# Kernel tuning notes

Hardware: AMD Instinct MI355X
Metric: run time of the kernel (lower is better)

Reference implementation:

```python
import jax, jax.numpy as jnp
import numpy as np
from jax import lax

B, L, D, F = 32, 512, 256, 256
K = 3
EPS = 1e-5


def _layer_norm(h, g, b):
    mu = jnp.mean(h, axis=-1, keepdims=True)
    var = jnp.var(h, axis=-1, keepdims=True)
    return (h - mu) * lax.rsqrt(var + EPS) * g + b


def _conv1d(h, w, b):
    # h: [B, L, Cin], w: [K, Cin, Cout] -> [B, L, Cout], 'same' padding (pad=1, k=3)
    return lax.conv_general_dilated(h, w, window_strides=(1,), padding=[(1, 1)],
                                    dimension_numbers=('NWC', 'WIO', 'NWC')) + b


def _duration_predictor(x, c1w, c1b, ln1g, ln1b, c2w, c2b, ln2g, ln2b, lw, lb):
    h = jax.nn.relu(_layer_norm(_conv1d(x, c1w, c1b), ln1g, ln1b))
    h = jax.nn.relu(_layer_norm(_conv1d(h, c2w, c2b), ln2g, ln2b))
    d = jax.nn.relu(h @ lw + lb)  # [B, L, 1]
    return d[..., 0]              # [B, L] (squeeze, training mode)


def _expand_one(xb, dur, M):
    # xb: [L, D], dur: [L] int. Repeat row i dur[i] times, zero-pad to M frames.
    cs = jnp.cumsum(dur)                              # [L]
    t = jnp.arange(M)                                 # [M]
    idx = jnp.searchsorted(cs, t, side='right')       # phoneme id per frame
    valid = t < cs[-1]
    out = jnp.take(xb, jnp.clip(idx, 0, xb.shape[0] - 1), axis=0)
    return jnp.where(valid[:, None], out, jnp.zeros((), xb.dtype))


def setup_inputs() -> dict:
    key = jax.random.key(0)
    ks = jax.random.split(key, 8)
    s_c = 1.0 / np.sqrt(K * F)
    s_l = 1.0 / np.sqrt(F)
    return {
        'x': jax.random.normal(ks[0], (B, L, D), jnp.float32),
        'durations': jax.random.randint(ks[1], (B, L), 0, 7),
        'mel_max_length': 4096,
        'conv1_w': jax.random.normal(ks[2], (K, D, F), jnp.float32) * s_c,
        'conv1_b': jnp.zeros((F,), jnp.float32),
        'ln1_g': jnp.ones((F,), jnp.float32),
        'ln1_b': jnp.zeros((F,), jnp.float32),
        'conv2_w': jax.random.normal(ks[3], (K, F, F), jnp.float32) * s_c,
        'conv2_b': jnp.zeros((F,), jnp.float32),
        'ln2_g': jnp.ones((F,), jnp.float32),
        'ln2_b': jnp.zeros((F,), jnp.float32),
        'lin_w': jax.random.normal(ks[4], (F, 1), jnp.float32) * s_l,
        'lin_b': jnp.zeros((1,), jnp.float32),
    }


def reference(x, durations, mel_max_length, conv1_w, conv1_b, ln1_g, ln1_b,
              conv2_w, conv2_b, ln2_g, ln2_b, lin_w, lin_b):
    dur_pred = _duration_predictor(x, conv1_w, conv1_b, ln1_g, ln1_b,
                                   conv2_w, conv2_b, ln2_g, ln2_b, lin_w, lin_b)
    dur = durations.astype(jnp.int32)
    output = jax.vmap(lambda xb, db: _expand_one(xb, db, mel_max_length))(x, dur)
    return output, dur_pred
```

## Files before the change

kernel.cpp:

```cpp
#include <hip/hip_runtime.h>

typedef __attribute__((ext_vector_type(8))) short short8;
typedef __attribute__((ext_vector_type(4))) float f32x4;

#define BATCH 32
#define LSEQ  512
#define DIN   256
#define FDIM  256
#define KTOT  768
#define MT    32
#define BK    32
#define PADA  264

__device__ __forceinline__ short f2bf(float f) {
    union { float f; unsigned u; } v; v.f = f;
    unsigned r = v.u + 0x7FFFu + ((v.u >> 16) & 1u);
    return (short)(r >> 16);
}

__global__ __launch_bounds__(512)
void prep_kernel(const int* __restrict__ dur, int* __restrict__ fidx, int M,
                 const float* __restrict__ w1, const float* __restrict__ w2,
                 short* __restrict__ wt1, short* __restrict__ wt2) {
    __shared__ int s[LSEQ];
    const int t = threadIdx.x, b = blockIdx.x;
    if (b < BATCH) {
        s[t] = dur[b * LSEQ + t];
        __syncthreads();
        for (int off = 1; off < LSEQ; off <<= 1) {
            int v = (t >= off) ? s[t - off] : 0;
            __syncthreads();
            s[t] += v;
            __syncthreads();
        }
        for (int f = t; f < M; f += 512) fidx[b * M + f] = -1;
        __syncthreads();
        int lo = (t == 0) ? 0 : s[t - 1];
        int hi = s[t];
        if (hi > M) hi = M;
        for (int j = lo; j < hi; j++) fidx[b * M + j] = b * LSEQ + t;
    } else {
        const int id = (b - BATCH) * 512 + t;
        const int n = id & 255, k = id >> 8;
        const int dst = (((k >> 5) * FDIM) + n) * BK + (k & 31);
        wt1[dst] = f2bf(w1[id]);
        wt2[dst] = f2bf(w2[id]);
    }
}

template<bool AF32, bool FUSE>
__global__ __launch_bounds__(256)
void conv_ln_expand(const void* __restrict__ Asrc, const short* __restrict__ Bt,
                    const float* __restrict__ cb, const float* __restrict__ g,
                    const float* __restrict__ bta, const float* __restrict__ lw,
                    const float* __restrict__ lb, short* __restrict__ Hout,
                    float* __restrict__ Dout,
                    const float4* __restrict__ x4, const int* __restrict__ fidx,
                    float4* __restrict__ out4, int M, int nexp, int ebase)
{
    __shared__ short As[34][PADA];
    __shared__ float redS[MT][4];
    __shared__ float redQ[MT][4];
    __shared__ float redD[MT][4];
    __shared__ float muS[MT];
    __shared__ float rsS[MT];

    const int tid  = threadIdx.x;
    const int lane = tid & 63;

    if (blockIdx.x < (unsigned)nexp) {
        const int fr = (ebase + blockIdx.x) * 4 + (tid >> 6);
        const int idx = fidx[fr];
        const size_t obase = (size_t)fr * 64 + lane;
        if (idx >= 0) out4[obase] = x4[(size_t)idx * 64 + lane];
        else          out4[obase] = make_float4(0.f, 0.f, 0.f, 0.f);
        return;
    }

    const int cblk = blockIdx.x - nexp;
    const int wave = tid >> 6;
    const int ml   = lane & 15;
    const int q    = lane >> 4;
    const int row0 = cblk * MT;
    const int bb   = row0 >> 9;
    const int r0   = row0 & (LSEQ - 1);

    for (int idx = tid; idx < 34 * 32; idx += 256) {
        const int r = idx >> 5, part = idx & 31;
        const int l2 = r0 + r - 1;
        short8 v = {0, 0, 0, 0, 0, 0, 0, 0};
        if (l2 >= 0 && l2 < LSEQ) {
            const size_t off = ((size_t)(bb * LSEQ + l2)) * DIN + part * 8;
            if (AF32) {
                const float4* s4 = (const float4*)((const float*)Asrc + off);
                float4 u0 = s4[0], u1 = s4[1];
                v[0] = f2bf(u0.x); v[1] = f2bf(u0.y); v[2] = f2bf(u0.z); v[3] = f2bf(u0.w);
                v[4] = f2bf(u1.x); v[5] = f2bf(u1.y); v[6] = f2bf(u1.z); v[7] = f2bf(u1.w);
            } else {
                v = *(const short8*)((const short*)Asrc + off);
            }
        }
        *(short8*)&As[r][part * 8] = v;
    }
    __syncthreads();

    f32x4 acc[2][4];
    #pragma unroll
    for (int mt = 0; mt < 2; mt++)
        #pragma unroll
        for (int nt = 0; nt < 4; nt++)
            #pragma unroll
            for (int r = 0; r < 4; r++)
                acc[mt][nt][r] = 0.f;

    const short* bptr = Bt + (size_t)(wave * 64 + ml) * BK + q * 8;
    #pragma unroll 1
    for (int tap = 0; tap < 3; tap++) {
        #pragma unroll
        for (int cc = 0; cc < 8; cc++) {
            short8 af0 = *(const short8*)&As[ml + tap][cc * 32 + q * 8];
            short8 af1 = *(const short8*)&As[16 + ml + tap][cc * 32 + q * 8];
            short8 b0 = *(const short8*)(bptr + 0 * 16 * BK);
            short8 b1 = *(const short8*)(bptr + 1 * 16 * BK);
            short8 b2 = *(const short8*)(bptr + 2 * 16 * BK);
            short8 b3 = *(const short8*)(bptr + 3 * 16 * BK);
            bptr += FDIM * BK;
            acc[0][0] = __builtin_amdgcn_mfma_f32_16x16x32_bf16(af0, b0, acc[0][0], 0, 0, 0);
            acc[0][1] = __builtin_amdgcn_mfma_f32_16x16x32_bf16(af0, b1, acc[0][1], 0, 0, 0);
            acc[0][2] = __builtin_amdgcn_mfma_f32_16x16x32_bf16(af0, b2, acc[0][2], 0, 0, 0);
            acc[0][3] = __builtin_amdgcn_mfma_f32_16x16x32_bf16(af0, b3, acc[0][3], 0, 0, 0);
            acc[1][0] = __builtin_amdgcn_mfma_f32_16x16x32_bf16(af1, b0, acc[1][0], 0, 0, 0);
            acc[1][1] = __builtin_amdgcn_mfma_f32_16x16x32_bf16(af1, b1, acc[1][1], 0, 0, 0);
            acc[1][2] = __builtin_amdgcn_mfma_f32_16x16x32_bf16(af1, b2, acc[1][2], 0, 0, 0);
            acc[1][3] = __builtin_amdgcn_mfma_f32_16x16x32_bf16(af1, b3, acc[1][3], 0, 0, 0);
        }
    }

    float cbv[4], gv[4], bv[4], lwv[4];
    #pragma unroll
    for (int nt = 0; nt < 4; nt++) {
        const int col = wave * 64 + nt * 16 + ml;
        cbv[nt] = cb[col]; gv[nt] = g[col]; bv[nt] = bta[col];
        lwv[nt] = FUSE ? lw[col] : 0.f;
    }
    #pragma unroll
    for (int mt = 0; mt < 2; mt++)
        #pragma unroll
        for (int nt = 0; nt < 4; nt++)
            #pragma unroll
            for (int r = 0; r < 4; r++)
                acc[mt][nt][r] += cbv[nt];

    #pragma unroll
    for (int mt = 0; mt < 2; mt++)
        #pragma unroll
        for (int r = 0; r < 4; r++) {
            float ps = 0.f, pq = 0.f;
            #pragma unroll
            for (int nt = 0; nt < 4; nt++) { float v = acc[mt][nt][r]; ps += v; pq += v * v; }
            #pragma unroll
            for (int d = 1; d < 16; d <<= 1) { ps += __shfl_xor(ps, d); pq += __shfl_xor(pq, d); }
            if (ml == 0) { const int row = mt * 16 + q * 4 + r; redS[row][wave] = ps; redQ[row][wave] = pq; }
        }
    __syncthreads();
    if (tid < MT) {
        float S = 0.f, Q = 0.f;
        #pragma unroll
        for (int w = 0; w < 4; w++) { S += redS[tid][w]; Q += redQ[tid][w]; }
        const float mu  = S * (1.f / 256.f);
        const float var = Q * (1.f / 256.f) - mu * mu;
        muS[tid] = mu; rsS[tid] = rsqrtf(var + 1e-5f);
    }
    __syncthreads();

    if (!FUSE) {
        #pragma unroll
        for (int mt = 0; mt < 2; mt++)
            #pragma unroll
            for (int r = 0; r < 4; r++) {
                const int row = mt * 16 + q * 4 + r;
                const float mu = muS[row], rs = rsS[row];
                #pragma unroll
                for (int nt = 0; nt < 4; nt++) {
                    const int col = wave * 64 + nt * 16 + ml;
                    float v = (acc[mt][nt][r] - mu) * rs * gv[nt] + bv[nt];
                    v = fmaxf(v, 0.f);
                    Hout[(size_t)(row0 + row) * FDIM + col] = f2bf(v);
                }
            }
    } else {
        #pragma unroll
        for (int mt = 0; mt < 2; mt++)
            #pragma unroll
            for (int r = 0; r < 4; r++) {
                const int row = mt * 16 + q * 4 + r;
                const float mu = muS[row], rs = rsS[row];
                float pd = 0.f;
                #pragma unroll
                for (int nt = 0; nt < 4; nt++) {
                    float v = (acc[mt][nt][r] - mu) * rs * gv[nt] + bv[nt];
                    v = fmaxf(v, 0.f);
                    pd += v * lwv[nt];
                }
                #pragma unroll
                for (int d = 1; d < 16; d <<= 1) pd += __shfl_xor(pd, d);
                if (ml == 0) redD[row][wave] = pd;
            }
        __syncthreads();
        if (tid < MT) {
            float Dv = 0.f;
            #pragma unroll
            for (int w = 0; w < 4; w++) Dv += redD[tid][w];
            Dout[row0 + tid] = fmaxf(Dv + lb[0], 0.f);
        }
    }
}

extern "C" void kernel_launch(void* const* d_in, const int* in_sizes, int n_in,
                              void* d_out, int out_size, void* d_ws, size_t ws_size,
                              hipStream_t stream)
{
    const float* x   = (const float*)d_in[0];
    const int*   dur = (const int*)d_in[1];
    const float* c1w = (const float*)d_in[3];
    const float* c1b = (const float*)d_in[4];
    const float* g1  = (const float*)d_in[5];
    const float* b1  = (const float*)d_in[6];
    const float* c2w = (const float*)d_in[7];
    const float* c2b = (const float*)d_in[8];
    const float* g2  = (const float*)d_in[9];
    const float* b2  = (const float*)d_in[10];
    const float* lw  = (const float*)d_in[11];
    const float* lb  = (const float*)d_in[12];

    const int M = (out_size - BATCH * LSEQ) / (BATCH * DIN);
    float* out     = (float*)d_out;
    float* dur_out = out + (size_t)BATCH * M * DIN;

    char* ws   = (char*)d_ws;
    int*  fidx = (int*)ws;
    short* wt1 = (short*)(ws + (512 << 10));
    short* wt2 = (short*)(ws + (512 << 10) + (384 << 10));
    short* h1  = (short*)(ws + (512 << 10) + 2 * (384 << 10));

    const int NCONV = (BATCH * LSEQ) / MT;
    const int NEXP  = (BATCH * M) / 4;
    const int E1    = NEXP / 2;
    const int E2    = NEXP - E1;

    hipLaunchKernelGGL(prep_kernel, dim3(BATCH + (KTOT * FDIM) / 512), dim3(512), 0, stream,
                       dur, fidx, M, c1w, c2w, wt1, wt2);
    hipLaunchKernelGGL((conv_ln_expand<true, false>), dim3(E1 + NCONV), dim3(256), 0, stream,
                       (const void*)x, wt1, c1b, g1, b1, (const float*)nullptr, (const float*)nullptr,
                       h1, (float*)nullptr,
                       (const float4*)x, fidx, (float4*)d_out, M, E1, 0);
    hipLaunchKernelGGL((conv_ln_expand<false, true>), dim3(E2 + NCONV), dim3(256), 0, stream,
                       (const void*)h1, wt2, c2b, g2, b2, lw, lb,
                       (short*)nullptr, dur_out,
                       (const float4*)x, fidx, (float4*)d_out, M, E2, E1);
}
```

Before: 241.8 us.

## Split expand gather out of conv kernels into dedicated multi-row expand kernel

```diff
diff --git a/kernel.cpp b/kernel.cpp
--- a/kernel.cpp
+++ b/kernel.cpp
@@ -50,13 +50,11 @@
 
 template<bool AF32, bool FUSE>
 __global__ __launch_bounds__(256)
-void conv_ln_expand(const void* __restrict__ Asrc, const short* __restrict__ Bt,
-                    const float* __restrict__ cb, const float* __restrict__ g,
-                    const float* __restrict__ bta, const float* __restrict__ lw,
-                    const float* __restrict__ lb, short* __restrict__ Hout,
-                    float* __restrict__ Dout,
-                    const float4* __restrict__ x4, const int* __restrict__ fidx,
-                    float4* __restrict__ out4, int M, int nexp, int ebase)
+void conv_ln(const void* __restrict__ Asrc, const short* __restrict__ Bt,
+             const float* __restrict__ cb, const float* __restrict__ g,
+             const float* __restrict__ bta, const float* __restrict__ lw,
+             const float* __restrict__ lb, short* __restrict__ Hout,
+             float* __restrict__ Dout)
 {
     __shared__ short As[34][PADA];
     __shared__ float redS[MT][4];
@@ -66,22 +64,11 @@
     __shared__ float rsS[MT];
 
     const int tid  = threadIdx.x;
+    const int wave = tid >> 6;
     const int lane = tid & 63;
-
-    if (blockIdx.x < (unsigned)nexp) {
-        const int fr = (ebase + blockIdx.x) * 4 + (tid >> 6);
-        const int idx = fidx[fr];
-        const size_t obase = (size_t)fr * 64 + lane;
-        if (idx >= 0) out4[obase] = x4[(size_t)idx * 64 + lane];
-        else          out4[obase] = make_float4(0.f, 0.f, 0.f, 0.f);
-        return;
-    }
-
-    const int cblk = blockIdx.x - nexp;
-    const int wave = tid >> 6;
     const int ml   = lane & 15;
     const int q    = lane >> 4;
-    const int row0 = cblk * MT;
+    const int row0 = blockIdx.x * MT;
     const int bb   = row0 >> 9;
     const int r0   = row0 & (LSEQ - 1);
 
@@ -216,6 +203,28 @@
     }
 }
 
+__global__ __launch_bounds__(256)
+void expand_kernel(const float4* __restrict__ x4, const int* __restrict__ fidx,
+                   float4* __restrict__ out4) {
+    const int wave = threadIdx.x >> 6;
+    const int lane = threadIdx.x & 63;
+    const int fr0  = blockIdx.x * 16 + wave * 4;
+
+    int idx[4];
+    #pragma unroll
+    for (int j = 0; j < 4; j++) idx[j] = fidx[fr0 + j];
+
+    float4 v[4];
+    #pragma unroll
+    for (int j = 0; j < 4; j++) {
+        v[j] = make_float4(0.f, 0.f, 0.f, 0.f);
+        if (idx[j] >= 0) v[j] = x4[(size_t)idx[j] * 64 + lane];
+    }
+    #pragma unroll
+    for (int j = 0; j < 4; j++)
+        out4[(size_t)(fr0 + j) * 64 + lane] = v[j];
+}
+
 extern "C" void kernel_launch(void* const* d_in, const int* in_sizes, int n_in,
                               void* d_out, int out_size, void* d_ws, size_t ws_size,
                               hipStream_t stream)
@@ -243,19 +252,14 @@
     short* wt2 = (short*)(ws + (512 << 10) + (384 << 10));
     short* h1  = (short*)(ws + (512 << 10) + 2 * (384 << 10));
 
-    const int NCONV = (BATCH * LSEQ) / MT;
-    const int NEXP  = (BATCH * M) / 4;
-    const int E1    = NEXP / 2;
-    const int E2    = NEXP - E1;
-
     hipLaunchKernelGGL(prep_kernel, dim3(BATCH + (KTOT * FDIM) / 512), dim3(512), 0, stream,
                        dur, fidx, M, c1w, c2w, wt1, wt2);
-    hipLaunchKernelGGL((conv_ln_expand<true, false>), dim3(E1 + NCONV), dim3(256), 0, stream,
+    hipLaunchKernelGGL((conv_ln<true, false>), dim3((BATCH * LSEQ) / MT), dim3(256), 0, stream,
                        (const void*)x, wt1, c1b, g1, b1, (const float*)nullptr, (const float*)nullptr,
-                       h1, (float*)nullptr,
-                       (const float4*)x, fidx, (float4*)d_out, M, E1, 0);
-    hipLaunchKernelGGL((conv_ln_expand<false, true>), dim3(E2 + NCONV), dim3(256), 0, stream,
+                       h1, (float*)nullptr);
+    hipLaunchKernelGGL((conv_ln<false, true>), dim3((BATCH * LSEQ) / MT), dim3(256), 0, stream,
                        (const void*)h1, wt2, c2b, g2, b2, lw, lb,
-                       (short*)nullptr, dur_out,
-                       (const float4*)x, fidx, (float4*)d_out, M, E2, E1);
-}
+                       (short*)nullptr, dur_out);
+    hipLaunchKernelGGL(expand_kernel, dim3((BATCH * M) / 16), dim3(256), 0, stream,
+                       (const float4*)x, fidx, (float4*)d_out);
+}
```

New measurement: 205.5 us. 15.0% less time.
